# Kernel optimization log

Hardware: AMD Instinct MI355X
Metric: run time of the kernel (lower is better)

## Reference

```python
import jax, jax.numpy as jnp
import numpy as np

B, S, D = 4, 1024, 1024
H, DH = 16, 64
F = 4 * D
EPS = 1e-6


def _ln(x, scale, bias, axes=-1):
    mean = jnp.mean(x, axis=axes, keepdims=True)
    var = jnp.var(x, axis=axes, keepdims=True)
    return (x - mean) * jax.lax.rsqrt(var + EPS) * scale + bias


def setup_inputs() -> dict:
    key = jax.random.key(0)
    ks = jax.random.split(key, 20)
    sd = 1.0 / np.sqrt(D)
    sf = 1.0 / np.sqrt(F)
    inp = {
        'x': jax.random.normal(ks[0], (B, S, D), jnp.float32),
        'z': jax.random.normal(ks[1], (B, S, D), jnp.float32),
        'ln1_s': jnp.ones((D,), jnp.float32),
        'ln1_b': jnp.zeros((D,), jnp.float32),
        'Wq': jax.random.normal(ks[2], (D, D), jnp.float32) * sd,
        'bq': jnp.zeros((D,), jnp.float32),
        'Wk': jax.random.normal(ks[3], (D, D), jnp.float32) * sd,
        'bk': jnp.zeros((D,), jnp.float32),
        'Wv': jax.random.normal(ks[4], (D, D), jnp.float32) * sd,
        'bv': jnp.zeros((D,), jnp.float32),
        'qn_s': jnp.ones((H, DH), jnp.float32),
        'qn_b': jnp.zeros((H, DH), jnp.float32),
        'kn_s': jnp.ones((H, DH), jnp.float32),
        'kn_b': jnp.zeros((H, DH), jnp.float32),
        'Wo': jax.random.normal(ks[5], (D, D), jnp.float32) * sd,
        'bo': jnp.zeros((D,), jnp.float32),
        'ln2_s': jnp.ones((D,), jnp.float32),
        'ln2_b': jnp.zeros((D,), jnp.float32),
        'W1': jax.random.normal(ks[6], (D, F), jnp.float32) * sd,
        'b1': jnp.zeros((F,), jnp.float32),
        'W2': jax.random.normal(ks[7], (D, F), jnp.float32) * sd,
        'b2': jnp.zeros((F,), jnp.float32),
        'W3': jax.random.normal(ks[8], (F, D), jnp.float32) * sf,
        'b3': jnp.zeros((D,), jnp.float32),
    }
    return inp


def reference(x, z, ln1_s, ln1_b, Wq, bq, Wk, bk, Wv, bv, qn_s, qn_b, kn_s, kn_b,
              Wo, bo, ln2_s, ln2_b, W1, b1, W2, b2, W3, b3):
    # z is unused by the original module body
    x_skip = x
    xn = _ln(x, ln1_s, ln1_b)
    q = (xn @ Wq + bq).reshape(B, S, H, DH)
    k = (xn @ Wk + bk).reshape(B, S, H, DH)
    v = (xn @ Wv + bv).reshape(B, S, H, DH)
    # QK-norm: flax LayerNorm(feature_axes=(-2,-1)) still reduces over axis -1,
    # but carries (H, DH)-shaped scale/bias
    q = _ln(q, qn_s, qn_b)
    k = _ln(k, kn_s, kn_b)
    attn = jnp.einsum('bqhd,bkhd->bhqk', q, k) / jnp.sqrt(jnp.asarray(DH, q.dtype))
    attn = jax.nn.softmax(attn, axis=-1)
    out = jnp.einsum('bhqk,bkhd->bqhd', attn, v).reshape(B, S, D)
    x = x_skip + out @ Wo + bo
    x_skip = x
    xn = _ln(x, ln2_s, ln2_b)
    x1 = xn @ W1 + b1
    x2 = xn @ W2 + b2
    h = x1 * jax.nn.gelu(x2, approximate=True)  # GeGLU
    x = x_skip + h @ W3 + b3
    return x
```

## Files before the change

### kernel.cpp

```cpp
#include <hip/hip_runtime.h>

typedef unsigned short u16;
typedef __bf16  bfrag  __attribute__((ext_vector_type(8)));
typedef float   f32x4  __attribute__((ext_vector_type(4)));
typedef u16     u16x8  __attribute__((ext_vector_type(8)));
typedef u16     u16x4  __attribute__((ext_vector_type(4)));

__device__ __forceinline__ float bf2f(u16 u) {
    unsigned v = ((unsigned)u) << 16;
    return __builtin_bit_cast(float, v);
}
__device__ __forceinline__ u16 f2bf(float f) {
    unsigned x = __builtin_bit_cast(unsigned, f);
    unsigned r = (x + 0x7fffu + ((x >> 16) & 1u)) >> 16;
    return (u16)r;
}
__device__ __forceinline__ void g2l16(const u16* g, u16* l) {
    __builtin_amdgcn_global_load_lds((__attribute__((address_space(1))) void*)g,
                                     (__attribute__((address_space(3))) void*)l, 16, 0, 0);
}
__device__ __forceinline__ float gelu_tanh(float x) {
    float c = 1.5957691216057308f * (x + 0.044715f * x * x * x);
    return x * __frcp_rn(1.0f + __expf(-c));
}

__global__ __launch_bounds__(256) void wt_all(
        const float* __restrict__ Wq, const float* __restrict__ Wk,
        const float* __restrict__ Wv, const float* __restrict__ Wo,
        const float* __restrict__ W1, const float* __restrict__ W2,
        const float* __restrict__ W3,
        u16* __restrict__ WqkvT, u16* __restrict__ WoT,
        u16* __restrict__ W12T, u16* __restrict__ W3T) {
    int blk = blockIdx.x;
    const float* W; u16* Wt; int R, C, local;
    if (blk < 3072) {
        int w = blk >> 10; local = blk & 1023;
        W = (w == 0) ? Wq : (w == 1) ? Wk : Wv;
        Wt = WqkvT + (size_t)w * 1024 * 1024; R = 1024; C = 1024;
    } else if (blk < 4096) { W = Wo; Wt = WoT; R = 1024; C = 1024; local = blk - 3072; }
    else if (blk < 8192)   { W = W1; Wt = W12T; R = 1024; C = 4096; local = blk - 4096; }
    else if (blk < 12288)  { W = W2; Wt = W12T + (size_t)4096 * 1024; R = 1024; C = 4096; local = blk - 8192; }
    else                   { W = W3; Wt = W3T; R = 4096; C = 1024; local = blk - 12288; }
    int tiles_x = C >> 5;
    int c0 = (local % tiles_x) * 32, r0 = (local / tiles_x) * 32;

    __shared__ float tile[32][33];
    int tx = threadIdx.x & 31, ty = threadIdx.x >> 5;
#pragma unroll
    for (int i = 0; i < 32; i += 8)
        tile[ty + i][tx] = W[(size_t)(r0 + ty + i) * C + c0 + tx];
    __syncthreads();
#pragma unroll
    for (int i = 0; i < 32; i += 8)
        Wt[(size_t)(c0 + ty + i) * R + r0 + tx] = f2bf(tile[tx][ty + i]);
}

__global__ __launch_bounds__(256) void ln1024(const float* __restrict__ x,
                                              const float* __restrict__ s,
                                              const float* __restrict__ bi,
                                              u16* __restrict__ out) {
    int row = blockIdx.x, t = threadIdx.x;
    const float4* xr = (const float4*)(x + (size_t)row * 1024);
    float4 v = xr[t];
    float sum = v.x + v.y + v.z + v.w;
    float sq  = v.x * v.x + v.y * v.y + v.z * v.z + v.w * v.w;
#pragma unroll
    for (int off = 1; off < 64; off <<= 1) {
        sum += __shfl_xor(sum, off);
        sq  += __shfl_xor(sq,  off);
    }
    __shared__ float s1[4], s2[4];
    int wave = t >> 6;
    if ((t & 63) == 0) { s1[wave] = sum; s2[wave] = sq; }
    __syncthreads();
    sum = s1[0] + s1[1] + s1[2] + s1[3];
    sq  = s2[0] + s2[1] + s2[2] + s2[3];
    float mean = sum * (1.0f / 1024.0f);
    float var  = sq  * (1.0f / 1024.0f) - mean * mean;
    float inv  = rsqrtf(var + 1e-6f);
    float4 sc = ((const float4*)s)[t], bb = ((const float4*)bi)[t];
    u16x4 o;
    o[0] = f2bf((v.x - mean) * inv * sc.x + bb.x);
    o[1] = f2bf((v.y - mean) * inv * sc.y + bb.y);
    o[2] = f2bf((v.z - mean) * inv * sc.z + bb.z);
    o[3] = f2bf((v.w - mean) * inv * sc.w + bb.w);
    *(u16x4*)&out[(size_t)row * 1024 + t * 4] = o;
}

__global__ __launch_bounds__(256) void qknorm2(u16* __restrict__ qkv,
                                               const float* __restrict__ qn_s,
                                               const float* __restrict__ qn_b,
                                               const float* __restrict__ kn_s,
                                               const float* __restrict__ kn_b) {
    int gid  = blockIdx.x * 4 + (threadIdx.x >> 6);
    int lane = threadIdx.x & 63;
    int tok = gid >> 5, rem = gid & 31, z = rem >> 4, h = rem & 15;
    size_t base = (size_t)tok * 3072 + z * 1024 + h * 64;
    float v = bf2f(qkv[base + lane]);
    float sum = v, sq = v * v;
#pragma unroll
    for (int off = 1; off < 64; off <<= 1) {
        sum += __shfl_xor(sum, off);
        sq  += __shfl_xor(sq,  off);
    }
    float mean = sum * (1.0f / 64.0f);
    float var  = sq  * (1.0f / 64.0f) - mean * mean;
    float inv  = rsqrtf(var + 1e-6f);
    const float* s = z ? kn_s : qn_s;
    const float* b = z ? kn_b : qn_b;
    float post = z ? 1.0f : 0.125f;
    float o = ((v - mean) * inv * s[h * 64 + lane] + b[h * 64 + lane]) * post;
    qkv[base + lane] = f2bf(o);
}

#define BM 128
#define BK 32
template <int EPI, int BN_, int BSEL>
__global__ __launch_bounds__(256) void gemm_bt(const u16* __restrict__ A,
                                               const u16* __restrict__ Bt,
                                               const float* __restrict__ bias,
                                               const float* __restrict__ bias2,
                                               const float* __restrict__ bias3,
                                               const float* __restrict__ res,
                                               void* __restrict__ Cout,
                                               int M, int N, int K) {
    __shared__ u16 As[BM * BK];
    __shared__ u16 Bs[BN_ * BK];
    constexpr int MI = (BN_ == 128) ? 4 : 2;
    constexpr int NI = 4;
    int tid = threadIdx.x, wave = tid >> 6, lane = tid & 63;
    int quad = lane >> 4, l15 = lane & 15;
    int row0 = blockIdx.y * BM, col0 = blockIdx.x * BN_;
    int wr = (BN_ == 128) ? (wave >> 1) * 64 : wave * 32;
    int wc = (BN_ == 128) ? (wave & 1) * 64 : 0;
    int swz = ((lane & 3) ^ ((lane >> 2) & 3)) * 8;
    int rswz = (quad ^ (l15 & 3)) * 8;

    f32x4 acc[MI][NI] = {};

    const u16* gA = A + (size_t)(row0 + wave * 32 + (lane >> 2)) * K + swz;
    u16* lA = &As[wave * 32 * BK];
    const u16* gB;
    u16* lB;
    if (BN_ == 128) { gB = Bt + (size_t)(col0 + wave * 32 + (lane >> 2)) * K + swz; lB = &Bs[wave * 32 * BK]; }
    else            { gB = Bt + (size_t)(col0 + wave * 16 + (lane >> 2)) * K + swz; lB = &Bs[wave * 16 * BK]; }

    for (int k0 = 0; k0 < K; k0 += BK) {
        __syncthreads();
        g2l16(gA + k0,          lA);
        g2l16(gA + k0 + 16 * K, lA + 16 * BK);
        if (BN_ == 128) {
            g2l16(gB + k0,          lB);
            g2l16(gB + k0 + 16 * K, lB + 16 * BK);
        } else {
            g2l16(gB + k0, lB);
        }
        __syncthreads();
        bfrag af[MI], bf[NI];
#pragma unroll
        for (int mi = 0; mi < MI; mi++)
            af[mi] = *(const bfrag*)&As[(wr + mi * 16 + l15) * BK + rswz];
#pragma unroll
        for (int ni = 0; ni < NI; ni++)
            bf[ni] = *(const bfrag*)&Bs[(wc + ni * 16 + l15) * BK + rswz];
#pragma unroll
        for (int mi = 0; mi < MI; mi++)
#pragma unroll
            for (int ni = 0; ni < NI; ni++)
                acc[mi][ni] = __builtin_amdgcn_mfma_f32_16x16x32_bf16(
                    af[mi], bf[ni], acc[mi][ni], 0, 0, 0);
    }

    float bv[NI];
    int cols[NI];
#pragma unroll
    for (int ni = 0; ni < NI; ni++) {
        cols[ni] = col0 + wc + ni * 16 + l15;
        if (BSEL == 1) {
            int seg = cols[ni] >> 10;
            const float* bp = (seg == 0) ? bias : (seg == 1) ? bias2 : bias3;
            bv[ni] = bp[cols[ni] & 1023];
        } else {
            bv[ni] = bias[cols[ni]];
        }
    }
#pragma unroll
    for (int mi = 0; mi < MI; mi++) {
        int rbase = row0 + wr + mi * 16 + quad * 4;
#pragma unroll
        for (int r = 0; r < 4; r++) {
            int row = rbase + r;
#pragma unroll
            for (int ni = 0; ni < NI; ni++) {
                float val = acc[mi][ni][r] + bv[ni];
                size_t idx = (size_t)row * N + cols[ni];
                if (EPI == 1) {
                    ((u16*)Cout)[idx] = f2bf(val);
                } else {
                    ((float*)Cout)[idx] = val + res[idx];
                }
            }
        }
    }
}

__global__ __launch_bounds__(256, 2) void gemm_w12(const u16* __restrict__ A,
                                                   const u16* __restrict__ W12T,
                                                   const float* __restrict__ b1,
                                                   const float* __restrict__ b2,
                                                   u16* __restrict__ H) {
    __shared__ u16 As[128 * BK];
    __shared__ u16 B1s[128 * BK];
    __shared__ u16 B2s[128 * BK];
    int tid = threadIdx.x, wave = tid >> 6, lane = tid & 63;
    int quad = lane >> 4, l15 = lane & 15;
    int row0 = blockIdx.y * 128, col0 = blockIdx.x * 128;
    int wr = (wave >> 1) * 64, wc = (wave & 1) * 64;
    int swz = ((lane & 3) ^ ((lane >> 2) & 3)) * 8;
    int rswz = (quad ^ (l15 & 3)) * 8;

    f32x4 acc1[4][4] = {}, acc2[4][4] = {};

    const u16* gA  = A    + (size_t)(row0 + wave * 32 + (lane >> 2)) * 1024 + swz;
    const u16* gB1 = W12T + (size_t)(col0 + wave * 32 + (lane >> 2)) * 1024 + swz;
    const u16* gB2 = gB1  + (size_t)4096 * 1024;
    u16* lA  = &As [wave * 32 * BK];
    u16* lB1 = &B1s[wave * 32 * BK];
    u16* lB2 = &B2s[wave * 32 * BK];

    for (int k0 = 0; k0 < 1024; k0 += BK) {
        __syncthreads();
        g2l16(gA  + k0,             lA);
        g2l16(gA  + k0 + 16 * 1024, lA  + 16 * BK);
        g2l16(gB1 + k0,             lB1);
        g2l16(gB1 + k0 + 16 * 1024, lB1 + 16 * BK);
        g2l16(gB2 + k0,             lB2);
        g2l16(gB2 + k0 + 16 * 1024, lB2 + 16 * BK);
        __syncthreads();
        bfrag af[4], b1f[4], b2f[4];
#pragma unroll
        for (int mi = 0; mi < 4; mi++)
            af[mi] = *(const bfrag*)&As[(wr + mi * 16 + l15) * BK + rswz];
#pragma unroll
        for (int ni = 0; ni < 4; ni++) {
            b1f[ni] = *(const bfrag*)&B1s[(wc + ni * 16 + l15) * BK + rswz];
            b2f[ni] = *(const bfrag*)&B2s[(wc + ni * 16 + l15) * BK + rswz];
        }
#pragma unroll
        for (int mi = 0; mi < 4; mi++)
#pragma unroll
            for (int ni = 0; ni < 4; ni++) {
                acc1[mi][ni] = __builtin_amdgcn_mfma_f32_16x16x32_bf16(
                    af[mi], b1f[ni], acc1[mi][ni], 0, 0, 0);
                acc2[mi][ni] = __builtin_amdgcn_mfma_f32_16x16x32_bf16(
                    af[mi], b2f[ni], acc2[mi][ni], 0, 0, 0);
            }
    }

    float bv1[4], bv2[4];
    int cols[4];
#pragma unroll
    for (int ni = 0; ni < 4; ni++) {
        cols[ni] = col0 + wc + ni * 16 + l15;
        bv1[ni] = b1[cols[ni]];
        bv2[ni] = b2[cols[ni]];
    }
#pragma unroll
    for (int mi = 0; mi < 4; mi++) {
        int rbase = row0 + wr + mi * 16 + quad * 4;
#pragma unroll
        for (int r = 0; r < 4; r++) {
#pragma unroll
            for (int ni = 0; ni < 4; ni++) {
                float x1 = acc1[mi][ni][r] + bv1[ni];
                float x2 = acc2[mi][ni][r] + bv2[ni];
                H[(size_t)(rbase + r) * 4096 + cols[ni]] = f2bf(x1 * gelu_tanh(x2));
            }
        }
    }
}

__global__ __launch_bounds__(256) void gemm_splitk(const u16* __restrict__ A,
                                                   const u16* __restrict__ Bt,
                                                   u16* __restrict__ p0,
                                                   u16* __restrict__ p1,
                                                   u16* __restrict__ p2,
                                                   u16* __restrict__ p3) {
    const int K = 4096, N = 1024;
    __shared__ u16 As[128 * BK];
    __shared__ u16 Bs[128 * BK];
    int tid = threadIdx.x, wave = tid >> 6, lane = tid & 63;
    int quad = lane >> 4, l15 = lane & 15;
    int row0 = blockIdx.y * 128, col0 = blockIdx.x * 128;
    int kz = blockIdx.z;
    u16* P = (kz == 0) ? p0 : (kz == 1) ? p1 : (kz == 2) ? p2 : p3;
    int wr = (wave >> 1) * 64, wc = (wave & 1) * 64;
    int swz = ((lane & 3) ^ ((lane >> 2) & 3)) * 8;
    int rswz = (quad ^ (l15 & 3)) * 8;

    f32x4 acc[4][4] = {};

    const u16* gA = A  + (size_t)(row0 + wave * 32 + (lane >> 2)) * K + kz * 1024 + swz;
    const u16* gB = Bt + (size_t)(col0 + wave * 32 + (lane >> 2)) * K + kz * 1024 + swz;
    u16* lA = &As[wave * 32 * BK];
    u16* lB = &Bs[wave * 32 * BK];

    for (int k0 = 0; k0 < 1024; k0 += BK) {
        __syncthreads();
        g2l16(gA + k0,          lA);
        g2l16(gA + k0 + 16 * K, lA + 16 * BK);
        g2l16(gB + k0,          lB);
        g2l16(gB + k0 + 16 * K, lB + 16 * BK);
        __syncthreads();
        bfrag af[4], bf[4];
#pragma unroll
        for (int mi = 0; mi < 4; mi++)
            af[mi] = *(const bfrag*)&As[(wr + mi * 16 + l15) * BK + rswz];
#pragma unroll
        for (int ni = 0; ni < 4; ni++)
            bf[ni] = *(const bfrag*)&Bs[(wc + ni * 16 + l15) * BK + rswz];
#pragma unroll
        for (int mi = 0; mi < 4; mi++)
#pragma unroll
            for (int ni = 0; ni < 4; ni++)
                acc[mi][ni] = __builtin_amdgcn_mfma_f32_16x16x32_bf16(
                    af[mi], bf[ni], acc[mi][ni], 0, 0, 0);
    }

#pragma unroll
    for (int mi = 0; mi < 4; mi++) {
        int rbase = row0 + wr + mi * 16 + quad * 4;
#pragma unroll
        for (int r = 0; r < 4; r++)
#pragma unroll
            for (int ni = 0; ni < 4; ni++)
                P[(size_t)(rbase + r) * N + wc + col0 + ni * 16 + l15] =
                    f2bf(acc[mi][ni][r]);
    }
}

__global__ __launch_bounds__(256) void reduce4(const u16* __restrict__ p0,
                                               const u16* __restrict__ p1,
                                               const u16* __restrict__ p2,
                                               const u16* __restrict__ p3,
                                               const float* __restrict__ xmid,
                                               const float* __restrict__ b3,
                                               float* __restrict__ out) {
    size_t i = ((size_t)blockIdx.x * 256 + threadIdx.x) * 4;
    float4 xm = *(const float4*)&xmid[i];
    float4 bb = *(const float4*)&b3[i & 1023];
    u16x4 a0 = *(const u16x4*)&p0[i];
    u16x4 a1 = *(const u16x4*)&p1[i];
    u16x4 a2 = *(const u16x4*)&p2[i];
    u16x4 a3 = *(const u16x4*)&p3[i];
    float4 o;
    o.x = xm.x + bb.x + bf2f(a0[0]) + bf2f(a1[0]) + bf2f(a2[0]) + bf2f(a3[0]);
    o.y = xm.y + bb.y + bf2f(a0[1]) + bf2f(a1[1]) + bf2f(a2[1]) + bf2f(a3[1]);
    o.z = xm.z + bb.z + bf2f(a0[2]) + bf2f(a1[2]) + bf2f(a2[2]) + bf2f(a3[2]);
    o.w = xm.w + bb.w + bf2f(a0[3]) + bf2f(a1[3]) + bf2f(a2[3]) + bf2f(a3[3]);
    *(float4*)&out[i] = o;
}

#define LP 72
__global__ __launch_bounds__(256) void flash(const u16* __restrict__ qkv,
                                             u16* __restrict__ o) {
    int qt = blockIdx.x, h = blockIdx.y, b = blockIdx.z;
    int tid = threadIdx.x, wave = tid >> 6, lane = tid & 63;
    int quad = lane >> 4, l15 = lane & 15;

    __shared__ u16 Qs[128 * LP];
    __shared__ u16 Ks[64 * LP];
    __shared__ u16 Vt[64 * LP];
    __shared__ u16 Ps[128 * LP];

    {
        int row = tid >> 1, half = tid & 1;
        const u16* src = qkv + (size_t)(b * 1024 + qt * 128 + row) * 3072 + h * 64 + half * 32;
        u16* dst = &Qs[row * LP + half * 32];
#pragma unroll
        for (int i = 0; i < 4; i++)
            ((u16x8*)dst)[i] = ((const u16x8*)src)[i];
    }

    f32x4 accO[2][4] = {};
    float m_run[2][4], l_run[2][4];
#pragma unroll
    for (int rt = 0; rt < 2; rt++)
#pragma unroll
        for (int r = 0; r < 4; r++) { m_run[rt][r] = -1e30f; l_run[rt][r] = 0.0f; }

    for (int kt = 0; kt < 16; kt++) {
        __syncthreads();
        {
            int row = tid >> 2, seg = tid & 3;
            size_t gb = (size_t)(b * 1024 + kt * 64 + row) * 3072 + h * 64;
            const u16* ksrc = qkv + gb + 1024 + seg * 16;
            *(u16x8*)&Ks[row * LP + seg * 16]     = *(const u16x8*)ksrc;
            *(u16x8*)&Ks[row * LP + seg * 16 + 8] = *(const u16x8*)(ksrc + 8);
            const u16* vsrc = qkv + gb + 2048 + seg * 16;
            u16x8 v0 = *(const u16x8*)vsrc, v1 = *(const u16x8*)(vsrc + 8);
#pragma unroll
            for (int j = 0; j < 8; j++) Vt[(seg * 16 + j) * LP + row]     = v0[j];
#pragma unroll
            for (int j = 0; j < 8; j++) Vt[(seg * 16 + 8 + j) * LP + row] = v1[j];
        }
        __syncthreads();

        f32x4 accS[2][4] = {};
#pragma unroll
        for (int kk = 0; kk < 2; kk++) {
            bfrag aq[2];
#pragma unroll
            for (int rt = 0; rt < 2; rt++)
                aq[rt] = *(const bfrag*)&Qs[(wave * 32 + rt * 16 + l15) * LP + kk * 32 + quad * 8];
#pragma unroll
            for (int ct = 0; ct < 4; ct++) {
                bfrag bk = *(const bfrag*)&Ks[(ct * 16 + l15) * LP + kk * 32 + quad * 8];
                accS[0][ct] = __builtin_amdgcn_mfma_f32_16x16x32_bf16(aq[0], bk, accS[0][ct], 0, 0, 0);
                accS[1][ct] = __builtin_amdgcn_mfma_f32_16x16x32_bf16(aq[1], bk, accS[1][ct], 0, 0, 0);
            }
        }

#pragma unroll
        for (int rt = 0; rt < 2; rt++) {
#pragma unroll
            for (int r = 0; r < 4; r++) {
                float tmax = accS[rt][0][r];
#pragma unroll
                for (int ct = 1; ct < 4; ct++) tmax = fmaxf(tmax, accS[rt][ct][r]);
#pragma unroll
                for (int m = 1; m < 16; m <<= 1) tmax = fmaxf(tmax, __shfl_xor(tmax, m));
                float mnew  = fmaxf(m_run[rt][r], tmax);
                float alpha = __expf(m_run[rt][r] - mnew);
                float lsum = 0.0f;
                float p[4];
#pragma unroll
                for (int ct = 0; ct < 4; ct++) {
                    p[ct] = __expf(accS[rt][ct][r] - mnew);
                    lsum += p[ct];
                }
#pragma unroll
                for (int m = 1; m < 16; m <<= 1) lsum += __shfl_xor(lsum, m);
                l_run[rt][r] = l_run[rt][r] * alpha + lsum;
                m_run[rt][r] = mnew;
#pragma unroll
                for (int oc = 0; oc < 4; oc++) accO[rt][oc][r] *= alpha;
                int prow = wave * 32 + rt * 16 + quad * 4 + r;
#pragma unroll
                for (int ct = 0; ct < 4; ct++)
                    Ps[prow * LP + ct * 16 + l15] = f2bf(p[ct]);
            }
        }

#pragma unroll
        for (int kk = 0; kk < 2; kk++) {
            bfrag ap[2];
#pragma unroll
            for (int rt = 0; rt < 2; rt++)
                ap[rt] = *(const bfrag*)&Ps[(wave * 32 + rt * 16 + l15) * LP + kk * 32 + quad * 8];
#pragma unroll
            for (int oc = 0; oc < 4; oc++) {
                bfrag bv = *(const bfrag*)&Vt[(oc * 16 + l15) * LP + kk * 32 + quad * 8];
                accO[0][oc] = __builtin_amdgcn_mfma_f32_16x16x32_bf16(ap[0], bv, accO[0][oc], 0, 0, 0);
                accO[1][oc] = __builtin_amdgcn_mfma_f32_16x16x32_bf16(ap[1], bv, accO[1][oc], 0, 0, 0);
            }
        }
    }

#pragma unroll
    for (int rt = 0; rt < 2; rt++) {
#pragma unroll
        for (int r = 0; r < 4; r++) {
            int srow = qt * 128 + wave * 32 + rt * 16 + quad * 4 + r;
            float linv = 1.0f / l_run[rt][r];
#pragma unroll
            for (int oc = 0; oc < 4; oc++)
                o[(size_t)(b * 1024 + srow) * 1024 + h * 64 + oc * 16 + l15] =
                    f2bf(accO[rt][oc][r] * linv);
        }
    }
}

extern "C" void kernel_launch(void* const* d_in, const int* in_sizes, int n_in,
                              void* d_out, int out_size, void* d_ws, size_t ws_size,
                              hipStream_t stream) {
    const float* x     = (const float*)d_in[0];
    const float* ln1_s = (const float*)d_in[2];
    const float* ln1_b = (const float*)d_in[3];
    const float* Wq = (const float*)d_in[4];  const float* bq = (const float*)d_in[5];
    const float* Wk = (const float*)d_in[6];  const float* bk = (const float*)d_in[7];
    const float* Wv = (const float*)d_in[8];  const float* bv = (const float*)d_in[9];
    const float* qn_s = (const float*)d_in[10]; const float* qn_b = (const float*)d_in[11];
    const float* kn_s = (const float*)d_in[12]; const float* kn_b = (const float*)d_in[13];
    const float* Wo = (const float*)d_in[14]; const float* bo = (const float*)d_in[15];
    const float* ln2_s = (const float*)d_in[16]; const float* ln2_b = (const float*)d_in[17];
    const float* W1 = (const float*)d_in[18]; const float* b1 = (const float*)d_in[19];
    const float* W2 = (const float*)d_in[20]; const float* b2 = (const float*)d_in[21];
    const float* W3 = (const float*)d_in[22]; const float* b3 = (const float*)d_in[23];
    float* out = (float*)d_out;

    char* ws = (char*)d_ws;
    const size_t MB = (size_t)1 << 20;
    u16* WqkvT = (u16*)(ws + 0);
    u16* WoT   = (u16*)(ws + 6 * MB);
    u16* W12T  = (u16*)(ws + 8 * MB);
    u16* W3T   = (u16*)(ws + 24 * MB);
    u16* xn1   = (u16*)(ws + 32 * MB);
    u16* attn  = (u16*)(ws + 32 * MB);
    u16* xn2   = (u16*)(ws + 32 * MB);
    u16* qkv   = (u16*)(ws + 40 * MB);
    float* xmid = (float*)(ws + 40 * MB);
    u16* p3    = (u16*)(ws + 56 * MB);
    u16* h     = (u16*)(ws + 64 * MB);
    u16* p0    = (u16*)(ws + 0);
    u16* p1    = (u16*)(ws + 8 * MB);
    u16* p2    = (u16*)(ws + 16 * MB);

    dim3 blk(256);

    wt_all<<<16384, blk, 0, stream>>>(Wq, Wk, Wv, Wo, W1, W2, W3,
                                      WqkvT, WoT, W12T, W3T);

    ln1024<<<4096, blk, 0, stream>>>(x, ln1_s, ln1_b, xn1);

    gemm_bt<1, 128, 1><<<dim3(24, 32), blk, 0, stream>>>(
        xn1, WqkvT, bq, bk, bv, nullptr, qkv, 4096, 3072, 1024);

    qknorm2<<<32768, blk, 0, stream>>>(qkv, qn_s, qn_b, kn_s, kn_b);

    flash<<<dim3(8, 16, 4), blk, 0, stream>>>(qkv, attn);

    gemm_bt<2, 64, 0><<<dim3(16, 32), blk, 0, stream>>>(
        attn, WoT, bo, nullptr, nullptr, x, xmid, 4096, 1024, 1024);

    ln1024<<<4096, blk, 0, stream>>>(xmid, ln2_s, ln2_b, xn2);

    gemm_w12<<<dim3(32, 32), blk, 0, stream>>>(xn2, W12T, b1, b2, h);

    gemm_splitk<<<dim3(8, 32, 4), blk, 0, stream>>>(h, W3T, p0, p1, p2, p3);

    reduce4<<<4096, blk, 0, stream>>>(p0, p1, p2, p3, xmid, b3, out);
}
```

Before: 470.7 us.

## Fuse QK layer-norm into QKV GEMM epilogue and revise LDS swizzle

Removes the standalone qknorm2 kernel. The per-head Q/K layer-norm, plus the 1/8 query scaling, is now computed in a new EPI==4 epilogue of the QKV GEMM. Each wave's 64 output columns map to exactly one head, so the 64-element statistics come from register values reduced with 16-lane shuffles. This avoids a separate read-modify-write pass over the Q/K activations and one kernel launch. Separately, the LDS XOR swizzle formulas for global-to-LDS writes and fragment reads are changed in all three GEMM kernels, aiming to cut bank conflicts; if the write and read mappings do not match, the results would be wrong.

```diff
diff --git a/kernel.cpp b/kernel.cpp
--- a/kernel.cpp
+++ b/kernel.cpp
@@ -23,6 +23,9 @@
     float c = 1.5957691216057308f * (x + 0.044715f * x * x * x);
     return x * __frcp_rn(1.0f + __expf(-c));
 }
+
+#define SWZ(lane)  ((((lane) & 3) ^ (((lane) >> 3) & 3)) * 8)
+#define RSWZ(quad, l15)  ((((quad) ^ (((l15) >> 1) & 3))) * 8)
 
 __global__ __launch_bounds__(256) void wt_all(
         const float* __restrict__ Wq, const float* __restrict__ Wk,
@@ -87,32 +90,6 @@
     *(u16x4*)&out[(size_t)row * 1024 + t * 4] = o;
 }
 
-__global__ __launch_bounds__(256) void qknorm2(u16* __restrict__ qkv,
-                                               const float* __restrict__ qn_s,
-                                               const float* __restrict__ qn_b,
-                                               const float* __restrict__ kn_s,
-                                               const float* __restrict__ kn_b) {
-    int gid  = blockIdx.x * 4 + (threadIdx.x >> 6);
-    int lane = threadIdx.x & 63;
-    int tok = gid >> 5, rem = gid & 31, z = rem >> 4, h = rem & 15;
-    size_t base = (size_t)tok * 3072 + z * 1024 + h * 64;
-    float v = bf2f(qkv[base + lane]);
-    float sum = v, sq = v * v;
-#pragma unroll
-    for (int off = 1; off < 64; off <<= 1) {
-        sum += __shfl_xor(sum, off);
-        sq  += __shfl_xor(sq,  off);
-    }
-    float mean = sum * (1.0f / 64.0f);
-    float var  = sq  * (1.0f / 64.0f) - mean * mean;
-    float inv  = rsqrtf(var + 1e-6f);
-    const float* s = z ? kn_s : qn_s;
-    const float* b = z ? kn_b : qn_b;
-    float post = z ? 1.0f : 0.125f;
-    float o = ((v - mean) * inv * s[h * 64 + lane] + b[h * 64 + lane]) * post;
-    qkv[base + lane] = f2bf(o);
-}
-
 #define BM 128
 #define BK 32
 template <int EPI, int BN_, int BSEL>
@@ -122,6 +99,10 @@
                                                const float* __restrict__ bias2,
                                                const float* __restrict__ bias3,
                                                const float* __restrict__ res,
+                                               const float* __restrict__ qn_s,
+                                               const float* __restrict__ qn_b,
+                                               const float* __restrict__ kn_s,
+                                               const float* __restrict__ kn_b,
                                                void* __restrict__ Cout,
                                                int M, int N, int K) {
     __shared__ u16 As[BM * BK];
@@ -133,8 +114,8 @@
     int row0 = blockIdx.y * BM, col0 = blockIdx.x * BN_;
     int wr = (BN_ == 128) ? (wave >> 1) * 64 : wave * 32;
     int wc = (BN_ == 128) ? (wave & 1) * 64 : 0;
-    int swz = ((lane & 3) ^ ((lane >> 2) & 3)) * 8;
-    int rswz = (quad ^ (l15 & 3)) * 8;
+    int swz = SWZ(lane);
+    int rswz = RSWZ(quad, l15);
 
     f32x4 acc[MI][NI] = {};
 
@@ -184,6 +165,58 @@
             bv[ni] = bias[cols[ni]];
         }
     }
+
+    if (EPI == 4) {
+        int cbase = col0 + wc;
+        int z = cbase >> 10;
+        int hd = (cbase >> 6) & 15;
+        float post = (z == 0) ? 0.125f : 1.0f;
+        float sn[NI], bn[NI];
+        if (z < 2) {
+            const float* ns = (z == 0) ? qn_s : kn_s;
+            const float* nb = (z == 0) ? qn_b : kn_b;
+#pragma unroll
+            for (int ni = 0; ni < NI; ni++) {
+                sn[ni] = ns[hd * 64 + ni * 16 + l15];
+                bn[ni] = nb[hd * 64 + ni * 16 + l15];
+            }
+        }
+#pragma unroll
+        for (int mi = 0; mi < MI; mi++) {
+            int rbase = row0 + wr + mi * 16 + quad * 4;
+#pragma unroll
+            for (int r = 0; r < 4; r++) {
+                float v0 = acc[mi][0][r] + bv[0];
+                float v1 = acc[mi][1][r] + bv[1];
+                float v2 = acc[mi][2][r] + bv[2];
+                float v3 = acc[mi][3][r] + bv[3];
+                size_t rb = (size_t)(rbase + r) * N + cbase;
+                if (z == 2) {
+                    ((u16*)Cout)[rb + 0 * 16 + l15] = f2bf(v0);
+                    ((u16*)Cout)[rb + 1 * 16 + l15] = f2bf(v1);
+                    ((u16*)Cout)[rb + 2 * 16 + l15] = f2bf(v2);
+                    ((u16*)Cout)[rb + 3 * 16 + l15] = f2bf(v3);
+                } else {
+                    float s  = v0 + v1 + v2 + v3;
+                    float sq = v0 * v0 + v1 * v1 + v2 * v2 + v3 * v3;
+#pragma unroll
+                    for (int m = 1; m < 16; m <<= 1) {
+                        s  += __shfl_xor(s,  m);
+                        sq += __shfl_xor(sq, m);
+                    }
+                    float mean = s * (1.0f / 64.0f);
+                    float var  = sq * (1.0f / 64.0f) - mean * mean;
+                    float inv  = rsqrtf(var + 1e-6f);
+                    ((u16*)Cout)[rb + 0 * 16 + l15] = f2bf(((v0 - mean) * inv * sn[0] + bn[0]) * post);
+                    ((u16*)Cout)[rb + 1 * 16 + l15] = f2bf(((v1 - mean) * inv * sn[1] + bn[1]) * post);
+                    ((u16*)Cout)[rb + 2 * 16 + l15] = f2bf(((v2 - mean) * inv * sn[2] + bn[2]) * post);
+                    ((u16*)Cout)[rb + 3 * 16 + l15] = f2bf(((v3 - mean) * inv * sn[3] + bn[3]) * post);
+                }
+            }
+        }
+        return;
+    }
+
 #pragma unroll
     for (int mi = 0; mi < MI; mi++) {
         int rbase = row0 + wr + mi * 16 + quad * 4;
@@ -216,8 +249,8 @@
     int quad = lane >> 4, l15 = lane & 15;
     int row0 = blockIdx.y * 128, col0 = blockIdx.x * 128;
     int wr = (wave >> 1) * 64, wc = (wave & 1) * 64;
-    int swz = ((lane & 3) ^ ((lane >> 2) & 3)) * 8;
-    int rswz = (quad ^ (l15 & 3)) * 8;
+    int swz = SWZ(lane);
+    int rswz = RSWZ(quad, l15);
 
     f32x4 acc1[4][4] = {}, acc2[4][4] = {};
 
@@ -295,8 +328,8 @@
     int kz = blockIdx.z;
     u16* P = (kz == 0) ? p0 : (kz == 1) ? p1 : (kz == 2) ? p2 : p3;
     int wr = (wave >> 1) * 64, wc = (wave & 1) * 64;
-    int swz = ((lane & 3) ^ ((lane >> 2) & 3)) * 8;
-    int rswz = (quad ^ (l15 & 3)) * 8;
+    int swz = SWZ(lane);
+    int rswz = RSWZ(quad, l15);
 
     f32x4 acc[4][4] = {};
 
@@ -523,15 +556,15 @@
 
     ln1024<<<4096, blk, 0, stream>>>(x, ln1_s, ln1_b, xn1);
 
-    gemm_bt<1, 128, 1><<<dim3(24, 32), blk, 0, stream>>>(
-        xn1, WqkvT, bq, bk, bv, nullptr, qkv, 4096, 3072, 1024);
-
-    qknorm2<<<32768, blk, 0, stream>>>(qkv, qn_s, qn_b, kn_s, kn_b);
+    gemm_bt<4, 128, 1><<<dim3(24, 32), blk, 0, stream>>>(
+        xn1, WqkvT, bq, bk, bv, nullptr, qn_s, qn_b, kn_s, kn_b,
+        qkv, 4096, 3072, 1024);
 
     flash<<<dim3(8, 16, 4), blk, 0, stream>>>(qkv, attn);
 
     gemm_bt<2, 64, 0><<<dim3(16, 32), blk, 0, stream>>>(
-        attn, WoT, bo, nullptr, nullptr, x, xmid, 4096, 1024, 1024);
+        attn, WoT, bo, nullptr, nullptr, x, nullptr, nullptr, nullptr, nullptr,
+        xmid, 4096, 1024, 1024);
 
     ln1024<<<4096, blk, 0, stream>>>(xmid, ln2_s, ln2_b, xn2);
 
```

After: 452.2 us. -3.9%, faster.
